# Optimization experiments

Measured on AMD Instinct MI355X. Metric: run time of the kernel, lower is better.

Reference implementation:

```python
import jax, jax.numpy as jnp
import numpy as np

SEQ, D_IN, D_OUT = 8192, 1024, 1024


def setup_inputs() -> dict:
    key = jax.random.key(0)
    kx, kq, kk, kv = jax.random.split(key, 4)
    # torch nn.Linear weights have shape (out_features, in_features)
    s = 1.0 / np.sqrt(D_IN)
    return {
        "x": jax.random.normal(kx, (SEQ, D_IN), dtype=jnp.float32),
        "Wq": jax.random.uniform(kq, (D_OUT, D_IN), dtype=jnp.float32, minval=-s, maxval=s),
        "Wk": jax.random.uniform(kk, (D_OUT, D_IN), dtype=jnp.float32, minval=-s, maxval=s),
        "Wv": jax.random.uniform(kv, (D_OUT, D_IN), dtype=jnp.float32, minval=-s, maxval=s),
    }


def reference(x, Wq, Wk, Wv):
    # Linear (no bias): y = x @ W.T
    q = x @ Wq.T          # [S, D_OUT]
    k = x @ Wk.T          # [S, D_OUT]
    v = x @ Wv.T          # [S, D_OUT]
    scale = 1.0 / jnp.sqrt(jnp.asarray(k.shape[-1], dtype=x.dtype))
    scores = (q @ k.T) * scale            # [S, S]
    weights = jax.nn.softmax(scores, axis=-1)
    return weights @ v                    # [S, D_OUT]
```

## Files before the change

kernel.cpp:

```cpp
#include <hip/hip_runtime.h>
#include <hip/hip_bf16.h>
#include <stdint.h>


#define SEQ 8192
#define DMODEL 1024
#define LOG2E 1.44269504088896340736f
#define GROUP_M 8

typedef __bf16 bf16_t;
typedef __bf16 bf16x8 __attribute__((ext_vector_type(8)));
typedef float f32x4 __attribute__((ext_vector_type(4)));

__global__ __launch_bounds__(256)
void convert_f32_bf16(const float* __restrict__ in, bf16_t* __restrict__ out, long n) {
    long i = ((long)blockIdx.x * 256 + threadIdx.x) * 4;
    if (i + 3 < n) {
        const float4 v = *(const float4*)(in + i);
        union { ushort4 u; bf16_t b[4]; } p;
        p.b[0] = (bf16_t)v.x; p.b[1] = (bf16_t)v.y;
        p.b[2] = (bf16_t)v.z; p.b[3] = (bf16_t)v.w;
        *(ushort4*)(out + i) = p.u;
    }
}

__global__ __launch_bounds__(256)
void add_f32(float* __restrict__ out, const float* __restrict__ part, long n) {
    long i = ((long)blockIdx.x * 256 + threadIdx.x) * 4;
    if (i + 3 < n) {
        float4 a = *(const float4*)(out + i);
        const float4 b = *(const float4*)(part + i);
        a.x += b.x; a.y += b.y; a.z += b.z; a.w += b.w;
        *(float4*)(out + i) = a;
    }
}

__global__ __launch_bounds__(256)
void zero_f32(float* __restrict__ p, int n) {
    int i = blockIdx.x * 256 + threadIdx.x;
    if (i < n) p[i] = 0.0f;
}

template <typename OutT, int MODE>
__global__ __launch_bounds__(512, 2)
void gemm_hn(const bf16_t* __restrict__ A, const bf16_t* __restrict__ B,
             OutT* __restrict__ C0, OutT* __restrict__ C1,
             float* __restrict__ lsum,
             int M, int N, int Kps, int lda, int ldb, int ldc,
             long plane, int cshift, float alpha)
{
    __shared__ bf16_t As[128 * 64];
    __shared__ bf16_t Bs[256 * 64];

    const int tid  = threadIdx.x;
    const int wave = tid >> 6;
    const int lane = tid & 63;

    const int nbm = M >> 7, nbn = N >> 8;
    const int tiles = nbm * nbn;
    int bid = blockIdx.x;
    const int sid = bid / tiles;
    bid -= sid * tiles;
    const long kbase = (long)sid * Kps;
    OutT* __restrict__ C = sid ? C1 : C0;

    const int cpx = tiles >> 3;
    bid = (bid & 7) * cpx + (bid >> 3);

    const int per_group = GROUP_M * nbn;
    const int gid   = bid / per_group;
    const int rem   = bid - gid * per_group;
    const int first = gid * GROUP_M;
    const int gsz   = min(nbm - first, GROUP_M);
    const int bm    = first + rem % gsz;
    const int bn    = rem / gsz;
    const long row0 = (long)bm * 128;
    const long col0 = (long)bn * 256;

    const int wm = (wave >> 2) * 64;
    const int wn = (wave & 3) * 64;
    const int lr = lane & 15;
    const int lq = lane >> 4;

    const int rt = tid >> 3;
    const int sl = ((tid & 7) + rt) & 7;
    const bf16_t* pa = A + (row0 + rt) * (long)lda + kbase + sl * 8;
    const bf16_t* pb = B + (col0 + rt) * (long)ldb + kbase + sl * 8;

    const int p0  = (lq - lr) & 7;
    const int p1  = p0 ^ 4;
    const int oA0 = (wm + lr) * 64 + p0 * 8;
    const int oA1 = (wm + lr) * 64 + p1 * 8;
    const int oB0 = (wn + lr) * 64 + p0 * 8;
    const int oB1 = (wn + lr) * 64 + p1 * 8;

    f32x4 acc[4][4] = {};

    for (int k0 = 0; k0 < Kps; k0 += 64) {
        #pragma unroll
        for (int i = 0; i < 2; ++i) {
            const bf16_t* ga = pa + k0 + (long)i * 64 * lda;
            __builtin_amdgcn_global_load_lds(
                (const __attribute__((address_space(1))) uint32_t*)ga,
                (__attribute__((address_space(3))) uint32_t*)(As + i * 4096 + tid * 8),
                16, 0, 0);
        }
        #pragma unroll
        for (int i = 0; i < 4; ++i) {
            const bf16_t* gb = pb + k0 + (long)i * 64 * ldb;
            __builtin_amdgcn_global_load_lds(
                (const __attribute__((address_space(1))) uint32_t*)gb,
                (__attribute__((address_space(3))) uint32_t*)(Bs + i * 4096 + tid * 8),
                16, 0, 0);
        }
        __syncthreads();

        #pragma unroll
        for (int t = 0; t < 2; ++t) {
            bf16x8 af[4], bfr[4];
            const int oA = t ? oA1 : oA0;
            const int oB = t ? oB1 : oB0;
            #pragma unroll
            for (int mi = 0; mi < 4; ++mi)
                af[mi] = *(const bf16x8*)(As + oA + mi * 1024);
            #pragma unroll
            for (int ni = 0; ni < 4; ++ni)
                bfr[ni] = *(const bf16x8*)(Bs + oB + ni * 1024);
            #pragma unroll
            for (int mi = 0; mi < 4; ++mi)
                #pragma unroll
                for (int ni = 0; ni < 4; ++ni)
                    acc[mi][ni] = __builtin_amdgcn_mfma_f32_16x16x32_bf16(
                        af[mi], bfr[ni], acc[mi][ni], 0, 0, 0);
        }
        __syncthreads();
    }

    OutT* __restrict__ Cb = C + (col0 >> cshift) * plane;
    const int ccol0 = (int)(col0 & (((long)1 << cshift) - 1));

    if (MODE == 2) {
        #pragma unroll
        for (int mi = 0; mi < 4; ++mi)
            #pragma unroll
            for (int rg = 0; rg < 4; ++rg) {
                const long r = row0 + wm + mi * 16 + lq * 4 + rg;
                const float inv = 1.0f / lsum[r];
                #pragma unroll
                for (int ni = 0; ni < 4; ++ni) {
                    const int c = ccol0 + wn + ni * 16 + lr;
                    Cb[r * (long)ldc + c] = (OutT)(acc[mi][ni][rg] * inv);
                }
            }
    } else {
        #pragma unroll
        for (int mi = 0; mi < 4; ++mi)
            #pragma unroll
            for (int ni = 0; ni < 4; ++ni)
                #pragma unroll
                for (int rg = 0; rg < 4; ++rg) {
                    const long r = row0 + wm + mi * 16 + lq * 4 + rg;
                    const int  c = ccol0 + wn + ni * 16 + lr;
                    Cb[r * (long)ldc + c] = (OutT)(alpha * acc[mi][ni][rg]);
                }
    }
}

template <typename OutT, int MODE>
__global__ __launch_bounds__(256, 3)
void gemm32(const bf16_t* __restrict__ A, const bf16_t* __restrict__ B,
            OutT* __restrict__ C0, OutT* __restrict__ C1,
            float* __restrict__ lsum,
            int M, int N, int Kps, int lda, int ldb, int ldc,
            long plane, int cshift, float alpha)
{
    __shared__ bf16_t As[2][128 * 32];
    __shared__ bf16_t Bs[2][128 * 32];

    const int tid  = threadIdx.x;
    const int wave = tid >> 6;
    const int lane = tid & 63;

    const int nbm = M >> 7, nbn = N >> 7;
    const int tiles = nbm * nbn;
    int bid = blockIdx.x;
    const int sid = bid / tiles;
    bid -= sid * tiles;
    const long kbase = (long)sid * Kps;
    OutT* __restrict__ C = sid ? C1 : C0;

    const int cpx = tiles >> 3;
    bid = (bid & 7) * cpx + (bid >> 3);

    const int per_group = GROUP_M * nbn;
    const int gid   = bid / per_group;
    const int rem   = bid - gid * per_group;
    const int first = gid * GROUP_M;
    const int gsz   = min(nbm - first, GROUP_M);
    const int bm    = first + rem % gsz;
    const int bn    = rem / gsz;
    const long row0 = (long)bm * 128;
    const long col0 = (long)bn * 128;

    const int wm = (wave >> 1) * 64;
    const int wn = (wave & 1) * 64;
    const int lr = lane & 15;
    const int lq = lane >> 4;

    const int rt = tid >> 2;
    const int sl = ((tid & 3) + ((tid >> 3) & 3)) & 3;
    const bf16_t* pa = A + (row0 + rt) * (long)lda + kbase + sl * 8;
    const bf16_t* pb = B + (col0 + rt) * (long)ldb + kbase + sl * 8;

    const int p0  = (lq - ((lr >> 1) & 3)) & 3;
    const int oA  = (wm + lr) * 32 + p0 * 8;
    const int oB  = (wn + lr) * 32 + p0 * 8;

    const int nt = Kps >> 5;

    f32x4 acc[4][4] = {};

#define STG32(kt, bsel)                                                         \
    {                                                                           \
        _Pragma("unroll")                                                       \
        for (int i = 0; i < 2; ++i) {                                           \
            const bf16_t* ga = pa + (long)(kt) * 32 + (long)i * 64 * lda;       \
            const bf16_t* gb = pb + (long)(kt) * 32 + (long)i * 64 * ldb;       \
            __builtin_amdgcn_global_load_lds(                                   \
                (const __attribute__((address_space(1))) uint32_t*)ga,          \
                (__attribute__((address_space(3))) uint32_t*)(As[bsel] + (long)(i * 256 + tid) * 8), \
                16, 0, 0);                                                      \
            __builtin_amdgcn_global_load_lds(                                   \
                (const __attribute__((address_space(1))) uint32_t*)gb,          \
                (__attribute__((address_space(3))) uint32_t*)(Bs[bsel] + (long)(i * 256 + tid) * 8), \
                16, 0, 0);                                                      \
        }                                                                       \
    }

    STG32(0, 0);

    for (int t = 0; t < nt; ++t) {
        const int c = t & 1;
        const bf16_t* as = As[c];
        const bf16_t* bs = Bs[c];

        asm volatile("s_waitcnt vmcnt(0)" ::: "memory");
        __builtin_amdgcn_s_barrier();
        asm volatile("" ::: "memory");

        if (t + 1 < nt) STG32(t + 1, c ^ 1);

        bf16x8 af[4], bfr[4];
        #pragma unroll
        for (int mi = 0; mi < 4; ++mi)
            af[mi] = *(const bf16x8*)(as + oA + mi * 512);
        #pragma unroll
        for (int ni = 0; ni < 4; ++ni)
            bfr[ni] = *(const bf16x8*)(bs + oB + ni * 512);
        #pragma unroll
        for (int mi = 0; mi < 4; ++mi)
            #pragma unroll
            for (int ni = 0; ni < 4; ++ni)
                acc[mi][ni] = __builtin_amdgcn_mfma_f32_16x16x32_bf16(
                    af[mi], bfr[ni], acc[mi][ni], 0, 0, 0);
    }
#undef STG32

    OutT* __restrict__ Cb = C + (col0 >> cshift) * plane;
    const int ccol0 = (int)(col0 & (((long)1 << cshift) - 1));

    if (MODE == 1) {
        #pragma unroll
        for (int mi = 0; mi < 4; ++mi)
            #pragma unroll
            for (int rg = 0; rg < 4; ++rg) {
                const long r = row0 + wm + mi * 16 + lq * 4 + rg;
                float part = 0.f;
                #pragma unroll
                for (int ni = 0; ni < 4; ++ni) {
                    const int c = ccol0 + wn + ni * 16 + lr;
                    const float e = exp2f(alpha * acc[mi][ni][rg]);
                    part += e;
                    Cb[r * (long)ldc + c] = (OutT)e;
                }
                part += __shfl_xor(part, 1);
                part += __shfl_xor(part, 2);
                part += __shfl_xor(part, 4);
                part += __shfl_xor(part, 8);
                if (lr == 0) atomicAdd(&lsum[r], part);
            }
    } else {
        #pragma unroll
        for (int mi = 0; mi < 4; ++mi)
            #pragma unroll
            for (int ni = 0; ni < 4; ++ni)
                #pragma unroll
                for (int rg = 0; rg < 4; ++rg) {
                    const long r = row0 + wm + mi * 16 + lq * 4 + rg;
                    const int  c = ccol0 + wn + ni * 16 + lr;
                    Cb[r * (long)ldc + c] = (OutT)(alpha * acc[mi][ni][rg]);
                }
    }
}

__global__ __launch_bounds__(256)
void transpose_bf16(const bf16_t* __restrict__ in, bf16_t* __restrict__ out,
                    int R, int ldin, int ldout)
{
    __shared__ bf16_t tile[32][33];
    const int tx = threadIdx.x & 31;
    const int ty = threadIdx.x >> 5;
    const int c0 = blockIdx.x * 32;
    const int r0 = blockIdx.y * 32;
    #pragma unroll
    for (int j = 0; j < 32; j += 8)
        tile[ty + j][tx] = in[(long)(r0 + ty + j) * ldin + c0 + tx];
    __syncthreads();
    #pragma unroll
    for (int j = 0; j < 32; j += 8)
        out[(long)(c0 + ty + j) * ldout + r0 + tx] = tile[tx][ty + j];
}

extern "C" void kernel_launch(void* const* d_in, const int* in_sizes, int n_in,
                              void* d_out, int out_size, void* d_ws, size_t ws_size,
                              hipStream_t stream)
{
    const float* x  = (const float*)d_in[0];
    const float* Wq = (const float*)d_in[1];
    const float* Wk = (const float*)d_in[2];
    const float* Wv = (const float*)d_in[3];
    float* out = (float*)d_out;

    char* ws = (char*)d_ws;
    const long XN = (long)SEQ * DMODEL;
    const long WN = (long)DMODEL * DMODEL;
    const long SN = (long)SEQ * SEQ;

    bf16_t* xb   = (bf16_t*)ws;
    bf16_t* wcat = (bf16_t*)(ws + XN * 2);
    bf16_t* qb   = (bf16_t*)(ws + XN * 2 + WN * 6);
    bf16_t* kb   = qb + XN;
    bf16_t* vb   = qb + 2 * XN;
    bf16_t* Sb   = (bf16_t*)(ws + XN * 2 + WN * 6 + XN * 6);
    float*  pvp  = (float*)(ws + XN * 2 + WN * 6 + XN * 6 + SN * 2);
    float*  lsum = (float*)(ws + XN * 2 + WN * 6 + XN * 6 + SN * 2 + XN * 4);
    bf16_t* vtb  = xb;

    const size_t base_need = (size_t)(XN * 2 + WN * 6 + XN * 6 + SN * 2);
    const bool use_split = ws_size >= base_need + XN * 4 + SEQ * 4;
    if (!use_split) lsum = (float*)(ws + base_need);

    convert_f32_bf16<<<(int)(XN / 4 / 256), 256, 0, stream>>>(x,  xb, XN);
    convert_f32_bf16<<<(int)(WN / 4 / 256), 256, 0, stream>>>(Wq, wcat,          WN);
    convert_f32_bf16<<<(int)(WN / 4 / 256), 256, 0, stream>>>(Wk, wcat + WN,     WN);
    convert_f32_bf16<<<(int)(WN / 4 / 256), 256, 0, stream>>>(Wv, wcat + 2 * WN, WN);
    zero_f32<<<SEQ / 256, 256, 0, stream>>>(lsum, SEQ);

    dim3 blk256(256);
    dim3 blk512(512);
    gemm_hn<bf16_t, 0><<<(SEQ / 128) * (3 * DMODEL / 256), blk512, 0, stream>>>(
        xb, wcat, qb, qb, nullptr, SEQ, 3 * DMODEL, DMODEL,
        DMODEL, DMODEL, DMODEL, XN, 10, 1.0f);

    transpose_bf16<<<dim3(DMODEL / 32, SEQ / 32), blk256, 0, stream>>>(
        vb, vtb, SEQ, DMODEL, SEQ);

    gemm32<bf16_t, 1><<<(SEQ / 128) * (SEQ / 128), blk256, 0, stream>>>(
        qb, kb, Sb, Sb, lsum, SEQ, SEQ, DMODEL,
        DMODEL, DMODEL, SEQ, 0, 30, 0.03125f * LOG2E);

    if (use_split) {
        gemm_hn<float, 2><<<2 * (SEQ / 128) * (DMODEL / 256), blk512, 0, stream>>>(
            Sb, vtb, out, pvp, lsum, SEQ, DMODEL, SEQ / 2,
            SEQ, SEQ, DMODEL, 0, 30, 1.0f);
        add_f32<<<(int)(XN / 4 / 256), 256, 0, stream>>>(out, pvp, XN);
    } else {
        gemm_hn<float, 2><<<(SEQ / 128) * (DMODEL / 256), blk512, 0, stream>>>(
            Sb, vtb, out, out, lsum, SEQ, DMODEL, SEQ,
            SEQ, SEQ, DMODEL, 0, 30, 1.0f);
    }
}
```

Baseline: 458.9 us.

## Double-buffer gemm_hn LDS tiles with K=32 stages to overlap loads and MFMA

Replaces the single-buffered K=64 LDS tile in gemm_hn with two K=32 buffers. The next tile is prefetched via global_load_lds while the current one is consumed, using one barrier per step. The goal is to hide global-load latency behind MFMA work and drop the second barrier per iteration. In exchange there are twice as many barrier/waitcnt steps per K, each with less MFMA work to cover them, and a new swizzle pattern that could alter LDS bank conflicts.

```diff
diff --git a/kernel.cpp b/kernel.cpp
--- a/kernel.cpp
+++ b/kernel.cpp
@@ -49,8 +49,8 @@
              int M, int N, int Kps, int lda, int ldb, int ldc,
              long plane, int cshift, float alpha)
 {
-    __shared__ bf16_t As[128 * 64];
-    __shared__ bf16_t Bs[256 * 64];
+    __shared__ bf16_t As[2][128 * 32];
+    __shared__ bf16_t Bs[2][256 * 32];
 
     const int tid  = threadIdx.x;
     const int wave = tid >> 6;
@@ -82,59 +82,64 @@
     const int lr = lane & 15;
     const int lq = lane >> 4;
 
-    const int rt = tid >> 3;
-    const int sl = ((tid & 7) + rt) & 7;
+    const int rt = tid >> 2;
+    const int sl = ((tid & 3) + ((tid >> 3) & 3)) & 3;
     const bf16_t* pa = A + (row0 + rt) * (long)lda + kbase + sl * 8;
     const bf16_t* pb = B + (col0 + rt) * (long)ldb + kbase + sl * 8;
 
-    const int p0  = (lq - lr) & 7;
-    const int p1  = p0 ^ 4;
-    const int oA0 = (wm + lr) * 64 + p0 * 8;
-    const int oA1 = (wm + lr) * 64 + p1 * 8;
-    const int oB0 = (wn + lr) * 64 + p0 * 8;
-    const int oB1 = (wn + lr) * 64 + p1 * 8;
+    const int p0  = (lq - ((lr >> 1) & 3)) & 3;
+    const int oA  = (wm + lr) * 32 + p0 * 8;
+    const int oB  = (wn + lr) * 32 + p0 * 8;
+
+    const int nt = Kps >> 5;
 
     f32x4 acc[4][4] = {};
 
-    for (int k0 = 0; k0 < Kps; k0 += 64) {
-        #pragma unroll
-        for (int i = 0; i < 2; ++i) {
-            const bf16_t* ga = pa + k0 + (long)i * 64 * lda;
-            __builtin_amdgcn_global_load_lds(
-                (const __attribute__((address_space(1))) uint32_t*)ga,
-                (__attribute__((address_space(3))) uint32_t*)(As + i * 4096 + tid * 8),
-                16, 0, 0);
-        }
-        #pragma unroll
-        for (int i = 0; i < 4; ++i) {
-            const bf16_t* gb = pb + k0 + (long)i * 64 * ldb;
-            __builtin_amdgcn_global_load_lds(
-                (const __attribute__((address_space(1))) uint32_t*)gb,
-                (__attribute__((address_space(3))) uint32_t*)(Bs + i * 4096 + tid * 8),
-                16, 0, 0);
-        }
-        __syncthreads();
-
-        #pragma unroll
-        for (int t = 0; t < 2; ++t) {
-            bf16x8 af[4], bfr[4];
-            const int oA = t ? oA1 : oA0;
-            const int oB = t ? oB1 : oB0;
-            #pragma unroll
-            for (int mi = 0; mi < 4; ++mi)
-                af[mi] = *(const bf16x8*)(As + oA + mi * 1024);
+#define STGHN(kt, bsel)                                                         \
+    {                                                                           \
+        const bf16_t* ga = pa + (long)(kt) * 32;                                \
+        __builtin_amdgcn_global_load_lds(                                       \
+            (const __attribute__((address_space(1))) uint32_t*)ga,              \
+            (__attribute__((address_space(3))) uint32_t*)(As[bsel] + (long)tid * 8), \
+            16, 0, 0);                                                          \
+        _Pragma("unroll")                                                       \
+        for (int i = 0; i < 2; ++i) {                                           \
+            const bf16_t* gb = pb + (long)(kt) * 32 + (long)i * 128 * ldb;      \
+            __builtin_amdgcn_global_load_lds(                                   \
+                (const __attribute__((address_space(1))) uint32_t*)gb,          \
+                (__attribute__((address_space(3))) uint32_t*)(Bs[bsel] + (long)(i * 512 + tid) * 8), \
+                16, 0, 0);                                                      \
+        }                                                                       \
+    }
+
+    STGHN(0, 0);
+
+    for (int t = 0; t < nt; ++t) {
+        const int c = t & 1;
+        const bf16_t* as = As[c];
+        const bf16_t* bs = Bs[c];
+
+        asm volatile("s_waitcnt vmcnt(0)" ::: "memory");
+        __builtin_amdgcn_s_barrier();
+        asm volatile("" ::: "memory");
+
+        if (t + 1 < nt) STGHN(t + 1, c ^ 1);
+
+        bf16x8 af[4], bfr[4];
+        #pragma unroll
+        for (int mi = 0; mi < 4; ++mi)
+            af[mi] = *(const bf16x8*)(as + oA + mi * 512);
+        #pragma unroll
+        for (int ni = 0; ni < 4; ++ni)
+            bfr[ni] = *(const bf16x8*)(bs + oB + ni * 512);
+        #pragma unroll
+        for (int mi = 0; mi < 4; ++mi)
             #pragma unroll
             for (int ni = 0; ni < 4; ++ni)
-                bfr[ni] = *(const bf16x8*)(Bs + oB + ni * 1024);
-            #pragma unroll
-            for (int mi = 0; mi < 4; ++mi)
-                #pragma unroll
-                for (int ni = 0; ni < 4; ++ni)
-                    acc[mi][ni] = __builtin_amdgcn_mfma_f32_16x16x32_bf16(
-                        af[mi], bfr[ni], acc[mi][ni], 0, 0, 0);
-        }
-        __syncthreads();
-    }
+                acc[mi][ni] = __builtin_amdgcn_mfma_f32_16x16x32_bf16(
+                    af[mi], bfr[ni], acc[mi][ni], 0, 0, 0);
+    }
+#undef STGHN
 
     OutT* __restrict__ Cb = C + (col0 >> cshift) * plane;
     const int ccol0 = (int)(col0 & (((long)1 << cshift) - 1));
```

After: 484.9 us. 5.7% more time.
